# Optimization experiments

Hardware: AMD Instinct MI355X
Metric: run time of the kernel (lower is better)

Reference implementation:

```python
import jax, jax.numpy as jnp
import numpy as np

B, N, FD, HD, MD, FS, NM = 8, 64, 128, 256, 64, 80, 6
D = HD + MD  # 320: GNN/decoder operating dim (fixes dim bug in original)
H = W = 128

def _mlp2(x, W1, b1, W2, b2):
    return jax.nn.relu(jax.nn.relu(x @ W1 + b1) @ W2 + b2)

def _forward(object_features, object_attributes, perception_features, object_positions,
             enc_W1, enc_b1, enc_W2, enc_b2, conv1_W, conv1_b, conv2_W, conv2_b,
             edge_W1, edge_b1, edge_W2, edge_b2, gru_Wih, gru_Whh, gru_bih, gru_bhh,
             mode_W1, mode_b1, mode_W2, mode_b2, traj_W1, traj_b1, traj_W2, traj_b2):
    # object encoder: [B,N,FD+8] -> [B,N,HD]
    obj_in = jnp.concatenate([object_features, object_attributes], -1)
    emb = _mlp2(obj_in, enc_W1, enc_b1, enc_W2, enc_b2)
    # map encoder (original discards result via random sampler; kept for faithfulness)
    dn = ('NCHW', 'OIHW', 'NCHW')
    m = jax.nn.relu(jax.lax.conv_general_dilated(perception_features, conv1_W, (1, 1), 'SAME', dimension_numbers=dn) + conv1_b[None, :, None, None])
    m = jax.nn.relu(jax.lax.conv_general_dilated(m, conv2_W, (1, 1), 'SAME', dimension_numbers=dn) + conv2_b[None, :, None, None])
    # sample_map_at_positions returns randn in the original; fixed-seed equivalent
    sampled = jax.random.normal(jax.random.key(42), (B, N, MD), dtype=emb.dtype)
    ctx = jnp.concatenate([emb, sampled], -1)  # [B,N,D]
    # Social GNN, fully vectorized over the ego-node loop i:
    rel = object_positions[:, :, None, :] - object_positions[:, None, :, :]  # [B,N,N,2] = pos[i]-pos[j]
    ego = jnp.broadcast_to(ctx[:, :, None, :], (B, N, N, D))
    nbr = jnp.broadcast_to(ctx[:, None, :, :], (B, N, N, D))
    e = _mlp2(jnp.concatenate([ego, nbr, rel], -1), edge_W1, edge_b1, edge_W2, edge_b2)  # [B,N,N,D]
    mask = (1.0 - jnp.eye(N, dtype=e.dtype))[None, :, :, None]
    agg = (e * mask).sum(2) / (N - 1 + 1e-10)  # [B,N,D]
    # GRUCell(input=concat(ctx,agg), hidden=ctx), torch semantics
    x = jnp.concatenate([ctx, agg], -1)  # [B,N,2D]
    gi = x @ gru_Wih + gru_bih
    gh = ctx @ gru_Whh + gru_bhh
    ir, iz, inn = jnp.split(gi, 3, -1)
    hr, hz, hn = jnp.split(gh, 3, -1)
    r = jax.nn.sigmoid(ir + hr)
    z = jax.nn.sigmoid(iz + hz)
    n = jnp.tanh(inn + r * hn)
    h = (1.0 - z) * n + z * ctx  # [B,N,D]
    # multi-modal trajectory decoder
    mode_probs = jax.nn.softmax(jax.nn.relu(h @ mode_W1 + mode_b1) @ mode_W2 + mode_b2, -1)  # [B,N,NM]
    t = jax.nn.relu(jnp.einsum('bnd,mde->bnme', h, traj_W1) + traj_b1)  # [B,N,NM,D]
    traj = jnp.einsum('bnme,mef->bnmf', t, traj_W2) + traj_b2  # [B,N,NM,FS*2]
    traj = traj.reshape(B, N, NM, FS, 2)
    return traj, mode_probs

def setup_inputs() -> dict:
    key = jax.random.key(0)
    ks = jax.random.split(key, 24)
    p = lambda k, shape: jax.random.normal(k, shape, dtype=jnp.float32) * 0.02
    z = lambda *shape: jnp.zeros(shape, dtype=jnp.float32)
    return {
        'object_features': jax.random.normal(ks[0], (B, N, FD), dtype=jnp.float32),
        'object_attributes': jax.random.normal(ks[1], (B, N, 8), dtype=jnp.float32),
        'perception_features': jax.random.normal(ks[2], (B, 256, H, W), dtype=jnp.float32),
        'object_positions': jax.random.normal(ks[3], (B, N, 2), dtype=jnp.float32),
        'enc_W1': p(ks[4], (FD + 8, HD)), 'enc_b1': z(HD),
        'enc_W2': p(ks[5], (HD, HD)), 'enc_b2': z(HD),
        'conv1_W': p(ks[6], (128, 256, 3, 3)), 'conv1_b': z(128),
        'conv2_W': p(ks[7], (64, 128, 3, 3)), 'conv2_b': z(64),
        'edge_W1': p(ks[8], (2 * D + 2, D)), 'edge_b1': z(D),
        'edge_W2': p(ks[9], (D, D)), 'edge_b2': z(D),
        'gru_Wih': p(ks[10], (2 * D, 3 * D)), 'gru_Whh': p(ks[11], (D, 3 * D)),
        'gru_bih': z(3 * D), 'gru_bhh': z(3 * D),
        'mode_W1': p(ks[12], (D, D)), 'mode_b1': z(D),
        'mode_W2': p(ks[13], (D, NM)), 'mode_b2': z(NM),
        'traj_W1': p(ks[14], (NM, D, D)), 'traj_b1': z(NM, D),
        'traj_W2': p(ks[15], (NM, D, FS * 2)), 'traj_b2': z(NM, FS * 2),
    }

def reference(object_features, object_attributes, perception_features, object_positions,
              enc_W1, enc_b1, enc_W2, enc_b2, conv1_W, conv1_b, conv2_W, conv2_b,
              edge_W1, edge_b1, edge_W2, edge_b2, gru_Wih, gru_Whh, gru_bih, gru_bhh,
              mode_W1, mode_b1, mode_W2, mode_b2, traj_W1, traj_b1, traj_W2, traj_b2):
    return _forward(object_features, object_attributes, perception_features, object_positions,
                    enc_W1, enc_b1, enc_W2, enc_b2, conv1_W, conv1_b, conv2_W, conv2_b,
                    edge_W1, edge_b1, edge_W2, edge_b2, gru_Wih, gru_Whh, gru_bih, gru_bhh,
                    mode_W1, mode_b1, mode_W2, mode_b2, traj_W1, traj_b1, traj_W2, traj_b2)
```

## Files before the change

kernel.cpp:

```cpp
#include <hip/hip_runtime.h>


typedef __attribute__((ext_vector_type(8))) short bf16x8;
typedef __attribute__((ext_vector_type(4))) float f32x4;

__device__ __forceinline__ unsigned short f2bf(float x) {
  unsigned u = __float_as_uint(x);
  return (unsigned short)((u + 0x7fffu + ((u >> 16) & 1u)) >> 16);
}

__device__ __forceinline__ void threefry2x32(unsigned k0, unsigned k1,
                                             unsigned& x0, unsigned& x1) {
  const unsigned ks0 = k0, ks1 = k1, ks2 = k0 ^ k1 ^ 0x1BD11BDAu;
  x0 += ks0; x1 += ks1;
#define TFR(r) { x0 += x1; x1 = (x1 << (r)) | (x1 >> (32 - (r))); x1 ^= x0; }
  TFR(13) TFR(15) TFR(26) TFR(6)  x0 += ks1; x1 += ks2 + 1u;
  TFR(17) TFR(29) TFR(16) TFR(24) x0 += ks2; x1 += ks0 + 2u;
  TFR(13) TFR(15) TFR(26) TFR(6)  x0 += ks0; x1 += ks1 + 3u;
  TFR(17) TFR(29) TFR(16) TFR(24) x0 += ks1; x1 += ks2 + 4u;
  TFR(13) TFR(15) TFR(26) TFR(6)  x0 += ks2; x1 += ks0 + 5u;
#undef TFR
}

__device__ __forceinline__ float erfinv_xla(float x) {
  float w = -logf((1.0f - x) * (1.0f + x));
  float p;
  if (w < 5.0f) {
    w = w - 2.5f;
    p = 2.81022636e-08f;
    p = fmaf(p, w, 3.43273939e-07f);
    p = fmaf(p, w, -3.5233877e-06f);
    p = fmaf(p, w, -4.39150654e-06f);
    p = fmaf(p, w, 0.00021858087f);
    p = fmaf(p, w, -0.00125372503f);
    p = fmaf(p, w, -0.00417768164f);
    p = fmaf(p, w, 0.246640727f);
    p = fmaf(p, w, 1.50140941f);
  } else {
    w = sqrtf(w) - 3.0f;
    p = -0.000200214257f;
    p = fmaf(p, w, 0.000100950558f);
    p = fmaf(p, w, 0.00134934322f);
    p = fmaf(p, w, -0.00367342844f);
    p = fmaf(p, w, 0.00573950773f);
    p = fmaf(p, w, -0.0076224613f);
    p = fmaf(p, w, 0.00943887047f);
    p = fmaf(p, w, 1.00167406f);
    p = fmaf(p, w, 2.83297682f);
  }
  return p * x;
}

__device__ __forceinline__ float jax_normal42(unsigned idx) {
  unsigned x0 = 0u, x1 = idx;
  threefry2x32(0u, 42u, x0, x1);
  unsigned bits = x0 ^ x1;
  float f = __uint_as_float((bits >> 9) | 0x3f800000u) - 1.0f;
  const float lo = -0.99999994f;
  float u = fmaxf(lo, f * 2.0f + lo);
  return 1.41421356237f * erfinv_xla(u);
}

__global__ __launch_bounds__(256)
void k_cvt(const float* __restrict__ W2e, const float* __restrict__ Wih,
           const float* __restrict__ Whh, const float* __restrict__ T1,
           const float* __restrict__ T2, const float* __restrict__ EW1,
           const float* __restrict__ MW1, const float* __restrict__ MW2,
           unsigned short* __restrict__ ub) {
  const int id = blockIdx.x * 256 + threadIdx.x;
  if (id >= 282240) return;
  if (id >= 281600) {
    const int rem = id - 281600;
    const int g = rem >> 4, n = rem & 15;
    unsigned short v[8];
#pragma unroll
    for (int e = 0; e < 8; ++e) v[e] = (n < 6) ? f2bf(MW2[(g * 8 + e) * 6 + n]) : 0;
    ushort4* d = (ushort4*)&ub[2252800 + (size_t)rem * 8];
    d[0] = make_ushort4(v[0], v[1], v[2], v[3]);
    d[1] = make_ushort4(v[4], v[5], v[6], v[7]);
    return;
  }
  const float* src;
  unsigned short* dst;
  int rem, N;
  if (id < 12800)       { src = W2e; dst = ub;           rem = id;          N = 320; }
  else if (id < 89600)  { src = Wih; dst = ub + 102400;  rem = id - 12800;  N = 960; }
  else if (id < 128000) { src = Whh; dst = ub + 716800;  rem = id - 89600;  N = 960; }
  else if (id < 204800) { src = T1;  dst = ub + 1024000; rem = id - 128000; N = 320; }
  else if (id < 243200) { src = T2;  dst = ub + 1638400; rem = id - 204800; N = 160; }
  else if (id < 268800) { src = EW1; dst = ub + 1945600; rem = id - 243200; N = 320; }
  else                  { src = MW1; dst = ub + 2150400; rem = id - 268800; N = 320; }
  const int g = rem / N, n = rem - g * N;
  const float* s = src + g * 8 * N + n;
  unsigned short v[8];
#pragma unroll
  for (int e = 0; e < 8; ++e) v[e] = f2bf(s[e * N]);
  ushort4* d = (ushort4*)&dst[(size_t)rem * 8];
  d[0] = make_ushort4(v[0], v[1], v[2], v[3]);
  d[1] = make_ushort4(v[4], v[5], v[6], v[7]);
}

__global__ __launch_bounds__(256)
void k_encoder(const float* __restrict__ feat, const float* __restrict__ attr,
               const float* __restrict__ W1, const float* __restrict__ b1,
               const float* __restrict__ W2, const float* __restrict__ b2,
               float* __restrict__ ctx) {
  __shared__ float s_in[4][136];
  __shared__ float s_h1[4][256];
  const int r0 = blockIdx.x * 4;
  const int t = threadIdx.x;
  for (int r = 0; r < 4; ++r) {
    if (t < 128)      s_in[r][t] = feat[(r0 + r) * 128 + t];
    else if (t < 136) s_in[r][t] = attr[(r0 + r) * 8 + (t - 128)];
  }
  __syncthreads();
  float acc[4];
#pragma unroll
  for (int r = 0; r < 4; ++r) acc[r] = b1[t];
  for (int k = 0; k < 136; ++k) {
    const float w = W1[k * 256 + t];
#pragma unroll
    for (int r = 0; r < 4; ++r) acc[r] = fmaf(s_in[r][k], w, acc[r]);
  }
#pragma unroll
  for (int r = 0; r < 4; ++r) s_h1[r][t] = fmaxf(acc[r], 0.0f);
  __syncthreads();
#pragma unroll
  for (int r = 0; r < 4; ++r) acc[r] = b2[t];
  for (int k = 0; k < 256; ++k) {
    const float w = W2[k * 256 + t];
#pragma unroll
    for (int r = 0; r < 4; ++r) acc[r] = fmaf(s_h1[r][k], w, acc[r]);
  }
#pragma unroll
  for (int r = 0; r < 4; ++r) ctx[(r0 + r) * 320 + t] = fmaxf(acc[r], 0.0f);
  if (t < 64) {
    for (int r = 0; r < 4; ++r)
      ctx[(r0 + r) * 320 + 256 + t] = jax_normal42((unsigned)((r0 + r) * 64 + t));
  }
}

__global__ __launch_bounds__(256)
void k_pqM(const float* __restrict__ ctx, const unsigned short* __restrict__ Bf,
           const float* __restrict__ b1, float* __restrict__ P,
           float* __restrict__ Q) {
  __shared__ __align__(16) unsigned short s_c[40 * 16 * 8];
  const int row0 = blockIdx.x * 16;
  const int half = blockIdx.y;
  const int t = threadIdx.x;
#pragma unroll
  for (int it = 0; it < 3; ++it) {
    const int idx = t + it * 256;
    if (idx < 640) {
      const int row = idx / 40, oct = idx - row * 40;
      const float4 v0 = *(const float4*)&ctx[(row0 + row) * 320 + oct * 8];
      const float4 v1 = *(const float4*)&ctx[(row0 + row) * 320 + oct * 8 + 4];
      ushort4* dst = (ushort4*)&s_c[(oct * 16 + row) * 8];
      dst[0] = make_ushort4(f2bf(v0.x), f2bf(v0.y), f2bf(v0.z), f2bf(v0.w));
      dst[1] = make_ushort4(f2bf(v1.x), f2bf(v1.y), f2bf(v1.z), f2bf(v1.w));
    }
  }
  __syncthreads();

  const int w = t >> 6, l = t & 63, lg = l >> 4, lr = l & 15;
  f32x4 acc[5];
#pragma unroll
  for (int u = 0; u < 5; ++u) acc[u] = (f32x4){0.f, 0.f, 0.f, 0.f};
#pragma unroll
  for (int ks = 0; ks < 10; ++ks) {
    const bf16x8 afr = *(const bf16x8*)&s_c[((ks * 4 + lg) * 16 + lr) * 8];
    bf16x8 bfr[5];
#pragma unroll
    for (int u = 0; u < 5; ++u)
      bfr[u] = *(const bf16x8*)&Bf[(((ks * 4 + lg) * 640) + half * 320 +
                                    w * 80 + u * 16 + lr) * 8];
#pragma unroll
    for (int u = 0; u < 5; ++u)
      acc[u] = __builtin_amdgcn_mfma_f32_16x16x32_bf16(afr, bfr[u], acc[u], 0, 0, 0);
  }
#pragma unroll
  for (int u = 0; u < 5; ++u) {
    const int n = w * 80 + u * 16 + lr;
    const float bias = (half == 0) ? b1[n] : 0.0f;
    float* dst = (half == 0) ? P : Q;
#pragma unroll
    for (int r = 0; r < 4; ++r) {
      const int row = row0 + lg * 4 + r;
      dst[row * 320 + n] = acc[u][r] + bias;
    }
  }
}

__global__ __launch_bounds__(256)
void k_edge(const float* __restrict__ P, const float* __restrict__ Q,
            const float* __restrict__ pos, const float* __restrict__ W1,
            const unsigned short* __restrict__ Bf, const float* __restrict__ b2,
            float* __restrict__ agg) {
  __shared__ __align__(16) unsigned short s_A[40 * 64 * 8];
  const int bx = blockIdx.x;
  const int b = bx >> 6, i = bx & 63;
  const int t = threadIdx.x;
  const int w = t >> 6, l = t & 63;

  {
    const int j = t & 63;
    const int sub = t >> 6;
    const float2 pi = *(const float2*)&pos[b * 128 + 2 * i];
    const float2 pj = *(const float2*)&pos[b * 128 + 2 * j];
    const float rx = pi.x - pj.x, ry = pi.y - pj.y;
    const float* __restrict__ Prow = P + bx * 320;
    const float* __restrict__ Qrow = Q + (b * 64 + j) * 320;
    const float* __restrict__ w0 = W1 + 640 * 320;
    const float* __restrict__ w1 = W1 + 641 * 320;
#pragma unroll
    for (int g = 0; g < 10; ++g) {
      const int k0 = g * 32 + sub * 8;
      const float4 p0 = *(const float4*)&Prow[k0];
      const float4 p1 = *(const float4*)&Prow[k0 + 4];
      const float4 q0 = *(const float4*)&Qrow[k0];
      const float4 q1 = *(const float4*)&Qrow[k0 + 4];
      const float4 a0 = *(const float4*)&w0[k0];
      const float4 a1 = *(const float4*)&w0[k0 + 4];
      const float4 c0 = *(const float4*)&w1[k0];
      const float4 c1 = *(const float4*)&w1[k0 + 4];
      float v[8];
      v[0] = fmaf(ry, c0.x, fmaf(rx, a0.x, p0.x + q0.x));
      v[1] = fmaf(ry, c0.y, fmaf(rx, a0.y, p0.y + q0.y));
      v[2] = fmaf(ry, c0.z, fmaf(rx, a0.z, p0.z + q0.z));
      v[3] = fmaf(ry, c0.w, fmaf(rx, a0.w, p0.w + q0.w));
      v[4] = fmaf(ry, c1.x, fmaf(rx, a1.x, p1.x + q1.x));
      v[5] = fmaf(ry, c1.y, fmaf(rx, a1.y, p1.y + q1.y));
      v[6] = fmaf(ry, c1.z, fmaf(rx, a1.z, p1.z + q1.z));
      v[7] = fmaf(ry, c1.w, fmaf(rx, a1.w, p1.w + q1.w));
      unsigned short u[8];
#pragma unroll
      for (int e = 0; e < 8; ++e) u[e] = f2bf(fmaxf(v[e], 0.0f));
      ushort4* dst = (ushort4*)&s_A[((g * 4 + sub) * 64 + j) * 8];
      dst[0] = make_ushort4(u[0], u[1], u[2], u[3]);
      dst[1] = make_ushort4(u[4], u[5], u[6], u[7]);
    }
  }
  __syncthreads();

  f32x4 acc[4][5];
#pragma unroll
  for (int mt = 0; mt < 4; ++mt)
#pragma unroll
    for (int u = 0; u < 5; ++u) acc[mt][u] = (f32x4){0.f, 0.f, 0.f, 0.f};

  const int lg = l >> 4, lr = l & 15;
  const unsigned short* __restrict__ Bbase = Bf + (lg * 320 + w * 80 + lr) * 8;
  const unsigned short* __restrict__ Abase = s_A + lg * 512 + lr * 8;

#pragma unroll 2
  for (int ks = 0; ks < 10; ++ks) {
    bf16x8 afr[4];
#pragma unroll
    for (int mt = 0; mt < 4; ++mt)
      afr[mt] = *(const bf16x8*)(Abase + ks * 2048 + mt * 128);
    bf16x8 bfr[5];
#pragma unroll
    for (int u = 0; u < 5; ++u)
      bfr[u] = *(const bf16x8*)(Bbase + ks * 10240 + u * 128);
#pragma unroll
    for (int mt = 0; mt < 4; ++mt)
#pragma unroll
      for (int u = 0; u < 5; ++u)
        acc[mt][u] = __builtin_amdgcn_mfma_f32_16x16x32_bf16(
            afr[mt], bfr[u], acc[mt][u], 0, 0, 0);
  }

#pragma unroll
  for (int u = 0; u < 5; ++u) {
    const int n = w * 80 + u * 16 + lr;
    const float bias = b2[n];
    float p = 0.0f;
#pragma unroll
    for (int mt = 0; mt < 4; ++mt) {
#pragma unroll
      for (int r = 0; r < 4; ++r) {
        const int j = mt * 16 + lg * 4 + r;
        const float e = fmaxf(acc[mt][u][r] + bias, 0.0f);
        p += (j != i) ? e : 0.0f;
      }
    }
    p += __shfl_xor(p, 16);
    p += __shfl_xor(p, 32);
    if (l < 16) agg[bx * 320 + n] = p * (1.0f / 63.0f);
  }
}

__global__ __launch_bounds__(256)
void k_gruM(const float* __restrict__ ctx, const float* __restrict__ agg,
            const unsigned short* __restrict__ BfI,
            const unsigned short* __restrict__ BfH,
            const float* __restrict__ bih, const float* __restrict__ bhh,
            float* __restrict__ h) {
  __shared__ __align__(16) unsigned short s_x[80 * 16 * 8];
  const int rb = blockIdx.x / 5, db = blockIdx.x % 5;
  const int row0 = rb * 16, d0 = db * 64;
  const int t = threadIdx.x;

#pragma unroll
  for (int it = 0; it < 5; ++it) {
    const int idx = t + it * 256;
    const int row = idx / 80, oct = idx - row * 80;
    float4 v0, v1;
    if (oct < 40) {
      v0 = *(const float4*)&ctx[(row0 + row) * 320 + oct * 8];
      v1 = *(const float4*)&ctx[(row0 + row) * 320 + oct * 8 + 4];
    } else {
      v0 = *(const float4*)&agg[(row0 + row) * 320 + (oct - 40) * 8];
      v1 = *(const float4*)&agg[(row0 + row) * 320 + (oct - 40) * 8 + 4];
    }
    ushort4* dst = (ushort4*)&s_x[(oct * 16 + row) * 8];
    dst[0] = make_ushort4(f2bf(v0.x), f2bf(v0.y), f2bf(v0.z), f2bf(v0.w));
    dst[1] = make_ushort4(f2bf(v1.x), f2bf(v1.y), f2bf(v1.z), f2bf(v1.w));
  }
  __syncthreads();

  const int w = t >> 6, l = t & 63, lg = l >> 4, lr = l & 15;
  const int d = d0 + w * 16 + lr;

  f32x4 accI[3], accH[3];
#pragma unroll
  for (int g = 0; g < 3; ++g) {
    accI[g] = (f32x4){0.f, 0.f, 0.f, 0.f};
    accH[g] = (f32x4){0.f, 0.f, 0.f, 0.f};
  }

#pragma unroll 2
  for (int ks = 0; ks < 20; ++ks) {
    const bf16x8 afr = *(const bf16x8*)&s_x[((ks * 4 + lg) * 16 + lr) * 8];
    bf16x8 bfr[3];
#pragma unroll
    for (int g = 0; g < 3; ++g)
      bfr[g] = *(const bf16x8*)&BfI[((ks * 4 + lg) * 960 + g * 320 + d) * 8];
#pragma unroll
    for (int g = 0; g < 3; ++g)
      accI[g] = __builtin_amdgcn_mfma_f32_16x16x32_bf16(afr, bfr[g], accI[g], 0, 0, 0);
  }
#pragma unroll 2
  for (int ks = 0; ks < 10; ++ks) {
    const bf16x8 afr = *(const bf16x8*)&s_x[((ks * 4 + lg) * 16 + lr) * 8];
    bf16x8 bfr[3];
#pragma unroll
    for (int g = 0; g < 3; ++g)
      bfr[g] = *(const bf16x8*)&BfH[((ks * 4 + lg) * 960 + g * 320 + d) * 8];
#pragma unroll
    for (int g = 0; g < 3; ++g)
      accH[g] = __builtin_amdgcn_mfma_f32_16x16x32_bf16(afr, bfr[g], accH[g], 0, 0, 0);
  }

  const float b_ir = bih[d], b_iz = bih[320 + d], b_in = bih[640 + d];
  const float b_hr = bhh[d], b_hz = bhh[320 + d], b_hn = bhh[640 + d];
#pragma unroll
  for (int r = 0; r < 4; ++r) {
    const int row = row0 + lg * 4 + r;
    const float ir = accI[0][r] + b_ir;
    const float iz = accI[1][r] + b_iz;
    const float inn = accI[2][r] + b_in;
    const float hr = accH[0][r] + b_hr;
    const float hz = accH[1][r] + b_hz;
    const float hn = accH[2][r] + b_hn;
    const float rr = 1.0f / (1.0f + expf(-(ir + hr)));
    const float zz = 1.0f / (1.0f + expf(-(iz + hz)));
    const float nn = tanhf(fmaf(rr, hn, inn));
    const float c = ctx[row * 320 + d];
    h[row * 320 + d] = (1.0f - zz) * nn + zz * c;
  }
}

__global__ __launch_bounds__(256)
void k_modeM(const float* __restrict__ h, const unsigned short* __restrict__ B1,
             const float* __restrict__ b1, const unsigned short* __restrict__ B2,
             const float* __restrict__ b2, float* __restrict__ out) {
  __shared__ __align__(16) unsigned short s_h[40 * 32 * 8];
  __shared__ __align__(16) unsigned short s_t[40 * 32 * 8];
  __shared__ float s_l[32][6];
  const int row0 = blockIdx.x * 32;
  const int t = threadIdx.x;

#pragma unroll
  for (int it = 0; it < 5; ++it) {
    const int idx = t + it * 256;
    const int row = idx / 40, oct = idx - row * 40;
    const float4 v0 = *(const float4*)&h[(row0 + row) * 320 + oct * 8];
    const float4 v1 = *(const float4*)&h[(row0 + row) * 320 + oct * 8 + 4];
    ushort4* dst = (ushort4*)&s_h[(oct * 32 + row) * 8];
    dst[0] = make_ushort4(f2bf(v0.x), f2bf(v0.y), f2bf(v0.z), f2bf(v0.w));
    dst[1] = make_ushort4(f2bf(v1.x), f2bf(v1.y), f2bf(v1.z), f2bf(v1.w));
  }
  __syncthreads();

  const int w = t >> 6, l = t & 63, lg = l >> 4, lr = l & 15;

  f32x4 acc1[2][5];
#pragma unroll
  for (int mt = 0; mt < 2; ++mt)
#pragma unroll
    for (int u = 0; u < 5; ++u) acc1[mt][u] = (f32x4){0.f, 0.f, 0.f, 0.f};
#pragma unroll
  for (int ks = 0; ks < 10; ++ks) {
    bf16x8 afr[2];
#pragma unroll
    for (int mt = 0; mt < 2; ++mt)
      afr[mt] = *(const bf16x8*)&s_h[(((ks * 4 + lg) * 32) + mt * 16 + lr) * 8];
    bf16x8 bfr[5];
#pragma unroll
    for (int u = 0; u < 5; ++u)
      bfr[u] = *(const bf16x8*)&B1[((ks * 4 + lg) * 320 + w * 80 + u * 16 + lr) * 8];
#pragma unroll
    for (int mt = 0; mt < 2; ++mt)
#pragma unroll
      for (int u = 0; u < 5; ++u)
        acc1[mt][u] = __builtin_amdgcn_mfma_f32_16x16x32_bf16(
            afr[mt], bfr[u], acc1[mt][u], 0, 0, 0);
  }
#pragma unroll
  for (int u = 0; u < 5; ++u) {
    const int n = w * 80 + u * 16 + lr;
    const float bias = b1[n];
#pragma unroll
    for (int mt = 0; mt < 2; ++mt) {
#pragma unroll
      for (int r = 0; r < 4; ++r) {
        const int row = mt * 16 + lg * 4 + r;
        s_t[((n >> 3) * 32 + row) * 8 + (n & 7)] =
            f2bf(fmaxf(acc1[mt][u][r] + bias, 0.0f));
      }
    }
  }
  __syncthreads();

  if (w < 2) {
    f32x4 acc2 = (f32x4){0.f, 0.f, 0.f, 0.f};
#pragma unroll
    for (int ks = 0; ks < 10; ++ks) {
      const bf16x8 afr = *(const bf16x8*)&s_t[(((ks * 4 + lg) * 32) + w * 16 + lr) * 8];
      const bf16x8 bfr = *(const bf16x8*)&B2[((ks * 4 + lg) * 16 + lr) * 8];
      acc2 = __builtin_amdgcn_mfma_f32_16x16x32_bf16(afr, bfr, acc2, 0, 0, 0);
    }
    if (lr < 6) {
#pragma unroll
      for (int r = 0; r < 4; ++r)
        s_l[w * 16 + lg * 4 + r][lr] = acc2[r] + b2[lr];
    }
  }
  __syncthreads();

  if (t < 32) {
    float v[6];
#pragma unroll
    for (int q = 0; q < 6; ++q) v[q] = s_l[t][q];
    float mx = v[0];
#pragma unroll
    for (int q = 1; q < 6; ++q) mx = fmaxf(mx, v[q]);
    float sum = 0.0f;
#pragma unroll
    for (int q = 0; q < 6; ++q) { v[q] = expf(v[q] - mx); sum += v[q]; }
    const float inv = 1.0f / sum;
#pragma unroll
    for (int q = 0; q < 6; ++q) out[491520 + (row0 + t) * 6 + q] = v[q] * inv;
  }
}

__global__ __launch_bounds__(256)
void k_trajM(const float* __restrict__ h, const unsigned short* __restrict__ B1,
             const float* __restrict__ b1, const unsigned short* __restrict__ B2,
             const float* __restrict__ b2, float* __restrict__ out) {
  __shared__ __align__(16) unsigned short s_h[40 * 16 * 8];
  __shared__ __align__(16) unsigned short s_t[40 * 16 * 8];
  const int rb = blockIdx.x, m = blockIdx.y;
  const int row0 = rb * 16;
  const int t = threadIdx.x;

#pragma unroll
  for (int it = 0; it < 3; ++it) {
    const int idx = t + it * 256;
    if (idx < 640) {
      const int row = idx / 40, oct = idx - row * 40;
      const float4 v0 = *(const float4*)&h[(row0 + row) * 320 + oct * 8];
      const float4 v1 = *(const float4*)&h[(row0 + row) * 320 + oct * 8 + 4];
      ushort4* dst = (ushort4*)&s_h[(oct * 16 + row) * 8];
      dst[0] = make_ushort4(f2bf(v0.x), f2bf(v0.y), f2bf(v0.z), f2bf(v0.w));
      dst[1] = make_ushort4(f2bf(v1.x), f2bf(v1.y), f2bf(v1.z), f2bf(v1.w));
    }
  }
  __syncthreads();

  const int w = t >> 6, l = t & 63, lg = l >> 4, lr = l & 15;

  f32x4 acc1[5];
#pragma unroll
  for (int u = 0; u < 5; ++u) acc1[u] = (f32x4){0.f, 0.f, 0.f, 0.f};
  const unsigned short* __restrict__ B1m = B1 + m * 102400;
#pragma unroll
  for (int ks = 0; ks < 10; ++ks) {
    const bf16x8 afr = *(const bf16x8*)&s_h[((ks * 4 + lg) * 16 + lr) * 8];
    bf16x8 bfr[5];
#pragma unroll
    for (int u = 0; u < 5; ++u)
      bfr[u] = *(const bf16x8*)&B1m[((ks * 4 + lg) * 320 + w * 80 + u * 16 + lr) * 8];
#pragma unroll
    for (int u = 0; u < 5; ++u)
      acc1[u] = __builtin_amdgcn_mfma_f32_16x16x32_bf16(afr, bfr[u], acc1[u], 0, 0, 0);
  }
#pragma unroll
  for (int u = 0; u < 5; ++u) {
    const int n = w * 80 + u * 16 + lr;
    const float bias = b1[m * 320 + n];
#pragma unroll
    for (int r = 0; r < 4; ++r) {
      const int row = lg * 4 + r;
      s_t[((n >> 3) * 16 + row) * 8 + (n & 7)] =
          f2bf(fmaxf(acc1[u][r] + bias, 0.0f));
    }
  }
  __syncthreads();

  const int nb = (w == 0) ? 0 : (w == 1) ? 3 : (w == 2) ? 6 : 7;
  f32x4 acc2[3];
#pragma unroll
  for (int u = 0; u < 3; ++u) acc2[u] = (f32x4){0.f, 0.f, 0.f, 0.f};
  const unsigned short* __restrict__ B2m = B2 + m * 51200;
#pragma unroll
  for (int ks = 0; ks < 10; ++ks) {
    const bf16x8 afr = *(const bf16x8*)&s_t[((ks * 4 + lg) * 16 + lr) * 8];
    bf16x8 bfr[3];
#pragma unroll
    for (int u = 0; u < 3; ++u)
      bfr[u] = *(const bf16x8*)&B2m[((ks * 4 + lg) * 160 + (nb + u) * 16 + lr) * 8];
#pragma unroll
    for (int u = 0; u < 3; ++u)
      acc2[u] = __builtin_amdgcn_mfma_f32_16x16x32_bf16(afr, bfr[u], acc2[u], 0, 0, 0);
  }
#pragma unroll
  for (int u = 0; u < 3; ++u) {
    const int n = (nb + u) * 16 + lr;
    const float bias = b2[m * 160 + n];
#pragma unroll
    for (int r = 0; r < 4; ++r) {
      const int row = row0 + lg * 4 + r;
      out[(row * 6 + m) * 160 + n] = acc2[u][r] + bias;
    }
  }
}

extern "C" void kernel_launch(void* const* d_in, const int* in_sizes, int n_in,
                              void* d_out, int out_size, void* d_ws, size_t ws_size,
                              hipStream_t stream) {
  (void)in_sizes; (void)n_in; (void)out_size; (void)ws_size;
  const float* feat  = (const float*)d_in[0];
  const float* attr  = (const float*)d_in[1];
  const float* pos   = (const float*)d_in[3];
  const float* encW1 = (const float*)d_in[4];
  const float* encb1 = (const float*)d_in[5];
  const float* encW2 = (const float*)d_in[6];
  const float* encb2 = (const float*)d_in[7];
  const float* edgW1 = (const float*)d_in[12];
  const float* edgb1 = (const float*)d_in[13];
  const float* edgW2 = (const float*)d_in[14];
  const float* edgb2 = (const float*)d_in[15];
  const float* Wih   = (const float*)d_in[16];
  const float* Whh   = (const float*)d_in[17];
  const float* bih   = (const float*)d_in[18];
  const float* bhh   = (const float*)d_in[19];
  const float* mW1   = (const float*)d_in[20];
  const float* mb1   = (const float*)d_in[21];
  const float* mW2   = (const float*)d_in[22];
  const float* mb2   = (const float*)d_in[23];
  const float* tW1   = (const float*)d_in[24];
  const float* tb1   = (const float*)d_in[25];
  const float* tW2   = (const float*)d_in[26];
  const float* tb2   = (const float*)d_in[27];

  float* out = (float*)d_out;
  float* ws  = (float*)d_ws;
  float* ctx  = ws;
  float* P    = ws + 163840;
  float* Q    = ws + 327680;
  float* agg  = ws + 491520;
  float* hbuf = ws + 655360;
  unsigned short* ub = (unsigned short*)(ws + 819200);
  unsigned short* W2bf  = ub;
  unsigned short* WihBf = ub + 102400;
  unsigned short* WhhBf = ub + 716800;
  unsigned short* T1bf  = ub + 1024000;
  unsigned short* T2bf  = ub + 1638400;
  unsigned short* EW1bf = ub + 1945600;
  unsigned short* MW1bf = ub + 2150400;
  unsigned short* MW2bf = ub + 2252800;

  k_cvt<<<1103, 256, 0, stream>>>(edgW2, Wih, Whh, tW1, tW2, edgW1, mW1, mW2, ub);
  k_encoder<<<128, 256, 0, stream>>>(feat, attr, encW1, encb1, encW2, encb2, ctx);
  k_pqM<<<dim3(32, 2), 256, 0, stream>>>(ctx, EW1bf, edgb1, P, Q);
  k_edge<<<512, 256, 0, stream>>>(P, Q, pos, edgW1, W2bf, edgb2, agg);
  k_gruM<<<160, 256, 0, stream>>>(ctx, agg, WihBf, WhhBf, bih, bhh, hbuf);
  k_modeM<<<16, 256, 0, stream>>>(hbuf, MW1bf, mb1, MW2bf, mb2, out);
  k_trajM<<<dim3(32, 6), 256, 0, stream>>>(hbuf, T1bf, tb1, T2bf, tb2, out);
}
```

Before: 87.48 us.

## Merge independent kernels and swizzle edge A-tile LDS layout

Merges the weight-conversion and encoder kernels into one launch, and the mode and trajectory head kernels into another. The goal is to cut launch overhead and let independent work run side by side. The edge kernel now fills its staging tile in a row-contiguous order that coalesces Q loads, and XOR-swizzles the shared-memory layout to reduce bank conflicts on the MFMA operand reads. The merged kernels share one shared-memory footprint sized for the larger branch, which may lower occupancy for the smaller branch.

```diff
diff --git a/kernel.cpp b/kernel.cpp
--- a/kernel.cpp
+++ b/kernel.cpp
@@ -62,53 +62,55 @@
 }
 
 __global__ __launch_bounds__(256)
-void k_cvt(const float* __restrict__ W2e, const float* __restrict__ Wih,
-           const float* __restrict__ Whh, const float* __restrict__ T1,
-           const float* __restrict__ T2, const float* __restrict__ EW1,
-           const float* __restrict__ MW1, const float* __restrict__ MW2,
-           unsigned short* __restrict__ ub) {
-  const int id = blockIdx.x * 256 + threadIdx.x;
-  if (id >= 282240) return;
-  if (id >= 281600) {
-    const int rem = id - 281600;
-    const int g = rem >> 4, n = rem & 15;
+void k_head(const float* __restrict__ W2e, const float* __restrict__ Wih,
+            const float* __restrict__ Whh, const float* __restrict__ T1,
+            const float* __restrict__ T2, const float* __restrict__ EW1,
+            const float* __restrict__ MW1, const float* __restrict__ MW2,
+            unsigned short* __restrict__ ub,
+            const float* __restrict__ feat, const float* __restrict__ attr,
+            const float* __restrict__ eW1, const float* __restrict__ eb1,
+            const float* __restrict__ eW2, const float* __restrict__ eb2,
+            float* __restrict__ ctx) {
+  __shared__ float s_in[4][136];
+  __shared__ float s_h1[4][256];
+  const int t = threadIdx.x;
+
+  if (blockIdx.x < 1103) {
+    const int id = blockIdx.x * 256 + t;
+    if (id >= 282240) return;
+    if (id >= 281600) {
+      const int rem = id - 281600;
+      const int g = rem >> 4, n = rem & 15;
+      unsigned short v[8];
+#pragma unroll
+      for (int e = 0; e < 8; ++e) v[e] = (n < 6) ? f2bf(MW2[(g * 8 + e) * 6 + n]) : 0;
+      ushort4* d = (ushort4*)&ub[2252800 + (size_t)rem * 8];
+      d[0] = make_ushort4(v[0], v[1], v[2], v[3]);
+      d[1] = make_ushort4(v[4], v[5], v[6], v[7]);
+      return;
+    }
+    const float* src;
+    unsigned short* dst;
+    int rem, N;
+    if (id < 12800)       { src = W2e; dst = ub;           rem = id;          N = 320; }
+    else if (id < 89600)  { src = Wih; dst = ub + 102400;  rem = id - 12800;  N = 960; }
+    else if (id < 128000) { src = Whh; dst = ub + 716800;  rem = id - 89600;  N = 960; }
+    else if (id < 204800) { src = T1;  dst = ub + 1024000; rem = id - 128000; N = 320; }
+    else if (id < 243200) { src = T2;  dst = ub + 1638400; rem = id - 204800; N = 160; }
+    else if (id < 268800) { src = EW1; dst = ub + 1945600; rem = id - 243200; N = 320; }
+    else                  { src = MW1; dst = ub + 2150400; rem = id - 268800; N = 320; }
+    const int g = rem / N, n = rem - g * N;
+    const float* s = src + g * 8 * N + n;
     unsigned short v[8];
 #pragma unroll
-    for (int e = 0; e < 8; ++e) v[e] = (n < 6) ? f2bf(MW2[(g * 8 + e) * 6 + n]) : 0;
-    ushort4* d = (ushort4*)&ub[2252800 + (size_t)rem * 8];
+    for (int e = 0; e < 8; ++e) v[e] = f2bf(s[e * N]);
+    ushort4* d = (ushort4*)&dst[(size_t)rem * 8];
     d[0] = make_ushort4(v[0], v[1], v[2], v[3]);
     d[1] = make_ushort4(v[4], v[5], v[6], v[7]);
     return;
   }
-  const float* src;
-  unsigned short* dst;
-  int rem, N;
-  if (id < 12800)       { src = W2e; dst = ub;           rem = id;          N = 320; }
-  else if (id < 89600)  { src = Wih; dst = ub + 102400;  rem = id - 12800;  N = 960; }
-  else if (id < 128000) { src = Whh; dst = ub + 716800;  rem = id - 89600;  N = 960; }
-  else if (id < 204800) { src = T1;  dst = ub + 1024000; rem = id - 128000; N = 320; }
-  else if (id < 243200) { src = T2;  dst = ub + 1638400; rem = id - 204800; N = 160; }
-  else if (id < 268800) { src = EW1; dst = ub + 1945600; rem = id - 243200; N = 320; }
-  else                  { src = MW1; dst = ub + 2150400; rem = id - 268800; N = 320; }
-  const int g = rem / N, n = rem - g * N;
-  const float* s = src + g * 8 * N + n;
-  unsigned short v[8];
-#pragma unroll
-  for (int e = 0; e < 8; ++e) v[e] = f2bf(s[e * N]);
-  ushort4* d = (ushort4*)&dst[(size_t)rem * 8];
-  d[0] = make_ushort4(v[0], v[1], v[2], v[3]);
-  d[1] = make_ushort4(v[4], v[5], v[6], v[7]);
-}
-
-__global__ __launch_bounds__(256)
-void k_encoder(const float* __restrict__ feat, const float* __restrict__ attr,
-               const float* __restrict__ W1, const float* __restrict__ b1,
-               const float* __restrict__ W2, const float* __restrict__ b2,
-               float* __restrict__ ctx) {
-  __shared__ float s_in[4][136];
-  __shared__ float s_h1[4][256];
-  const int r0 = blockIdx.x * 4;
-  const int t = threadIdx.x;
+
+  const int r0 = (blockIdx.x - 1103) * 4;
   for (int r = 0; r < 4; ++r) {
     if (t < 128)      s_in[r][t] = feat[(r0 + r) * 128 + t];
     else if (t < 136) s_in[r][t] = attr[(r0 + r) * 8 + (t - 128)];
@@ -116,9 +118,9 @@
   __syncthreads();
   float acc[4];
 #pragma unroll
-  for (int r = 0; r < 4; ++r) acc[r] = b1[t];
+  for (int r = 0; r < 4; ++r) acc[r] = eb1[t];
   for (int k = 0; k < 136; ++k) {
-    const float w = W1[k * 256 + t];
+    const float w = eW1[k * 256 + t];
 #pragma unroll
     for (int r = 0; r < 4; ++r) acc[r] = fmaf(s_in[r][k], w, acc[r]);
   }
@@ -126,9 +128,9 @@
   for (int r = 0; r < 4; ++r) s_h1[r][t] = fmaxf(acc[r], 0.0f);
   __syncthreads();
 #pragma unroll
-  for (int r = 0; r < 4; ++r) acc[r] = b2[t];
+  for (int r = 0; r < 4; ++r) acc[r] = eb2[t];
   for (int k = 0; k < 256; ++k) {
-    const float w = W2[k * 256 + t];
+    const float w = eW2[k * 256 + t];
 #pragma unroll
     for (int r = 0; r < 4; ++r) acc[r] = fmaf(s_h1[r][k], w, acc[r]);
   }
@@ -203,22 +205,23 @@
   const int w = t >> 6, l = t & 63;
 
   {
-    const int j = t & 63;
-    const int sub = t >> 6;
     const float2 pi = *(const float2*)&pos[b * 128 + 2 * i];
-    const float2 pj = *(const float2*)&pos[b * 128 + 2 * j];
-    const float rx = pi.x - pj.x, ry = pi.y - pj.y;
     const float* __restrict__ Prow = P + bx * 320;
-    const float* __restrict__ Qrow = Q + (b * 64 + j) * 320;
     const float* __restrict__ w0 = W1 + 640 * 320;
     const float* __restrict__ w1 = W1 + 641 * 320;
 #pragma unroll
-    for (int g = 0; g < 10; ++g) {
-      const int k0 = g * 32 + sub * 8;
+    for (int it = 0; it < 10; ++it) {
+      const int tau = w * 640 + it * 64 + l;
+      const int j = tau / 40;
+      const int oct = tau - j * 40;
+      const int k0 = oct * 8;
+      const float2 pj = *(const float2*)&pos[b * 128 + 2 * j];
+      const float rx = pi.x - pj.x, ry = pi.y - pj.y;
+      const float* __restrict__ Qrow = Q + (b * 64 + j) * 320;
+      const float4 q0 = *(const float4*)&Qrow[k0];
+      const float4 q1 = *(const float4*)&Qrow[k0 + 4];
       const float4 p0 = *(const float4*)&Prow[k0];
       const float4 p1 = *(const float4*)&Prow[k0 + 4];
-      const float4 q0 = *(const float4*)&Qrow[k0];
-      const float4 q1 = *(const float4*)&Qrow[k0 + 4];
       const float4 a0 = *(const float4*)&w0[k0];
       const float4 a1 = *(const float4*)&w0[k0 + 4];
       const float4 c0 = *(const float4*)&w1[k0];
@@ -235,9 +238,9 @@
       unsigned short u[8];
 #pragma unroll
       for (int e = 0; e < 8; ++e) u[e] = f2bf(fmaxf(v[e], 0.0f));
-      ushort4* dst = (ushort4*)&s_A[((g * 4 + sub) * 64 + j) * 8];
-      dst[0] = make_ushort4(u[0], u[1], u[2], u[3]);
-      dst[1] = make_ushort4(u[4], u[5], u[6], u[7]);
+      const int swz = ((oct * 64 + j) * 8) ^ ((oct & 7) << 3);
+      *(ushort4*)&s_A[swz]     = make_ushort4(u[0], u[1], u[2], u[3]);
+      *(ushort4*)&s_A[swz + 4] = make_ushort4(u[4], u[5], u[6], u[7]);
     }
   }
   __syncthreads();
@@ -250,14 +253,16 @@
 
   const int lg = l >> 4, lr = l & 15;
   const unsigned short* __restrict__ Bbase = Bf + (lg * 320 + w * 80 + lr) * 8;
-  const unsigned short* __restrict__ Abase = s_A + lg * 512 + lr * 8;
 
 #pragma unroll 2
   for (int ks = 0; ks < 10; ++ks) {
+    const int oct = ks * 4 + lg;
     bf16x8 afr[4];
 #pragma unroll
-    for (int mt = 0; mt < 4; ++mt)
-      afr[mt] = *(const bf16x8*)(Abase + ks * 2048 + mt * 128);
+    for (int mt = 0; mt < 4; ++mt) {
+      const int elem = ((oct * 64 + mt * 16 + lr) * 8) ^ ((oct & 7) << 3);
+      afr[mt] = *(const bf16x8*)&s_A[elem];
+    }
     bf16x8 bfr[5];
 #pragma unroll
     for (int u = 0; u < 5; ++u)
@@ -372,108 +377,108 @@
 }
 
 __global__ __launch_bounds__(256)
-void k_modeM(const float* __restrict__ h, const unsigned short* __restrict__ B1,
-             const float* __restrict__ b1, const unsigned short* __restrict__ B2,
-             const float* __restrict__ b2, float* __restrict__ out) {
-  __shared__ __align__(16) unsigned short s_h[40 * 32 * 8];
-  __shared__ __align__(16) unsigned short s_t[40 * 32 * 8];
+void k_tail(const float* __restrict__ h, const unsigned short* __restrict__ MB1,
+            const float* __restrict__ mb1, const unsigned short* __restrict__ MB2,
+            const float* __restrict__ mb2, const unsigned short* __restrict__ TB1,
+            const float* __restrict__ tb1, const unsigned short* __restrict__ TB2,
+            const float* __restrict__ tb2, float* __restrict__ out) {
+  __shared__ __align__(16) unsigned short s_buf[20480];
   __shared__ float s_l[32][6];
-  const int row0 = blockIdx.x * 32;
   const int t = threadIdx.x;
-
-#pragma unroll
-  for (int it = 0; it < 5; ++it) {
-    const int idx = t + it * 256;
-    const int row = idx / 40, oct = idx - row * 40;
-    const float4 v0 = *(const float4*)&h[(row0 + row) * 320 + oct * 8];
-    const float4 v1 = *(const float4*)&h[(row0 + row) * 320 + oct * 8 + 4];
-    ushort4* dst = (ushort4*)&s_h[(oct * 32 + row) * 8];
-    dst[0] = make_ushort4(f2bf(v0.x), f2bf(v0.y), f2bf(v0.z), f2bf(v0.w));
-    dst[1] = make_ushort4(f2bf(v1.x), f2bf(v1.y), f2bf(v1.z), f2bf(v1.w));
-  }
-  __syncthreads();
-
   const int w = t >> 6, l = t & 63, lg = l >> 4, lr = l & 15;
 
-  f32x4 acc1[2][5];
-#pragma unroll
-  for (int mt = 0; mt < 2; ++mt)
-#pragma unroll
-    for (int u = 0; u < 5; ++u) acc1[mt][u] = (f32x4){0.f, 0.f, 0.f, 0.f};
-#pragma unroll
-  for (int ks = 0; ks < 10; ++ks) {
-    bf16x8 afr[2];
+  if (blockIdx.x < 16) {
+    unsigned short* s_h = s_buf;
+    unsigned short* s_t = s_buf + 10240;
+    const int row0 = blockIdx.x * 32;
+#pragma unroll
+    for (int it = 0; it < 5; ++it) {
+      const int idx = t + it * 256;
+      const int row = idx / 40, oct = idx - row * 40;
+      const float4 v0 = *(const float4*)&h[(row0 + row) * 320 + oct * 8];
+      const float4 v1 = *(const float4*)&h[(row0 + row) * 320 + oct * 8 + 4];
+      ushort4* dst = (ushort4*)&s_h[(oct * 32 + row) * 8];
+      dst[0] = make_ushort4(f2bf(v0.x), f2bf(v0.y), f2bf(v0.z), f2bf(v0.w));
+      dst[1] = make_ushort4(f2bf(v1.x), f2bf(v1.y), f2bf(v1.z), f2bf(v1.w));
+    }
+    __syncthreads();
+
+    f32x4 acc1[2][5];
 #pragma unroll
     for (int mt = 0; mt < 2; ++mt)
-      afr[mt] = *(const bf16x8*)&s_h[(((ks * 4 + lg) * 32) + mt * 16 + lr) * 8];
-    bf16x8 bfr[5];
-#pragma unroll
-    for (int u = 0; u < 5; ++u)
-      bfr[u] = *(const bf16x8*)&B1[((ks * 4 + lg) * 320 + w * 80 + u * 16 + lr) * 8];
-#pragma unroll
-    for (int mt = 0; mt < 2; ++mt)
+#pragma unroll
+      for (int u = 0; u < 5; ++u) acc1[mt][u] = (f32x4){0.f, 0.f, 0.f, 0.f};
+#pragma unroll
+    for (int ks = 0; ks < 10; ++ks) {
+      bf16x8 afr[2];
+#pragma unroll
+      for (int mt = 0; mt < 2; ++mt)
+        afr[mt] = *(const bf16x8*)&s_h[(((ks * 4 + lg) * 32) + mt * 16 + lr) * 8];
+      bf16x8 bfr[5];
 #pragma unroll
       for (int u = 0; u < 5; ++u)
-        acc1[mt][u] = __builtin_amdgcn_mfma_f32_16x16x32_bf16(
-            afr[mt], bfr[u], acc1[mt][u], 0, 0, 0);
-  }
-#pragma unroll
-  for (int u = 0; u < 5; ++u) {
-    const int n = w * 80 + u * 16 + lr;
-    const float bias = b1[n];
-#pragma unroll
-    for (int mt = 0; mt < 2; ++mt) {
-#pragma unroll
-      for (int r = 0; r < 4; ++r) {
-        const int row = mt * 16 + lg * 4 + r;
-        s_t[((n >> 3) * 32 + row) * 8 + (n & 7)] =
-            f2bf(fmaxf(acc1[mt][u][r] + bias, 0.0f));
+        bfr[u] = *(const bf16x8*)&MB1[((ks * 4 + lg) * 320 + w * 80 + u * 16 + lr) * 8];
+#pragma unroll
+      for (int mt = 0; mt < 2; ++mt)
+#pragma unroll
+        for (int u = 0; u < 5; ++u)
+          acc1[mt][u] = __builtin_amdgcn_mfma_f32_16x16x32_bf16(
+              afr[mt], bfr[u], acc1[mt][u], 0, 0, 0);
+    }
+#pragma unroll
+    for (int u = 0; u < 5; ++u) {
+      const int n = w * 80 + u * 16 + lr;
+      const float bias = mb1[n];
+#pragma unroll
+      for (int mt = 0; mt < 2; ++mt) {
+#pragma unroll
+        for (int r = 0; r < 4; ++r) {
+          const int row = mt * 16 + lg * 4 + r;
+          s_t[((n >> 3) * 32 + row) * 8 + (n & 7)] =
+              f2bf(fmaxf(acc1[mt][u][r] + bias, 0.0f));
+        }
       }
     }
-  }
-  __syncthreads();
-
-  if (w < 2) {
-    f32x4 acc2 = (f32x4){0.f, 0.f, 0.f, 0.f};
-#pragma unroll
-    for (int ks = 0; ks < 10; ++ks) {
-      const bf16x8 afr = *(const bf16x8*)&s_t[(((ks * 4 + lg) * 32) + w * 16 + lr) * 8];
-      const bf16x8 bfr = *(const bf16x8*)&B2[((ks * 4 + lg) * 16 + lr) * 8];
-      acc2 = __builtin_amdgcn_mfma_f32_16x16x32_bf16(afr, bfr, acc2, 0, 0, 0);
-    }
-    if (lr < 6) {
-#pragma unroll
-      for (int r = 0; r < 4; ++r)
-        s_l[w * 16 + lg * 4 + r][lr] = acc2[r] + b2[lr];
-    }
-  }
-  __syncthreads();
-
-  if (t < 32) {
-    float v[6];
-#pragma unroll
-    for (int q = 0; q < 6; ++q) v[q] = s_l[t][q];
-    float mx = v[0];
-#pragma unroll
-    for (int q = 1; q < 6; ++q) mx = fmaxf(mx, v[q]);
-    float sum = 0.0f;
-#pragma unroll
-    for (int q = 0; q < 6; ++q) { v[q] = expf(v[q] - mx); sum += v[q]; }
-    const float inv = 1.0f / sum;
-#pragma unroll
-    for (int q = 0; q < 6; ++q) out[491520 + (row0 + t) * 6 + q] = v[q] * inv;
-  }
-}
-
-__global__ __launch_bounds__(256)
-void k_trajM(const float* __restrict__ h, const unsigned short* __restrict__ B1,
-             const float* __restrict__ b1, const unsigned short* __restrict__ B2,
-             const float* __restrict__ b2, float* __restrict__ out) {
-  __shared__ __align__(16) unsigned short s_h[40 * 16 * 8];
-  __shared__ __align__(16) unsigned short s_t[40 * 16 * 8];
-  const int rb = blockIdx.x, m = blockIdx.y;
+    __syncthreads();
+
+    if (w < 2) {
+      f32x4 acc2 = (f32x4){0.f, 0.f, 0.f, 0.f};
+#pragma unroll
+      for (int ks = 0; ks < 10; ++ks) {
+        const bf16x8 afr = *(const bf16x8*)&s_t[(((ks * 4 + lg) * 32) + w * 16 + lr) * 8];
+        const bf16x8 bfr = *(const bf16x8*)&MB2[((ks * 4 + lg) * 16 + lr) * 8];
+        acc2 = __builtin_amdgcn_mfma_f32_16x16x32_bf16(afr, bfr, acc2, 0, 0, 0);
+      }
+      if (lr < 6) {
+#pragma unroll
+        for (int r = 0; r < 4; ++r)
+          s_l[w * 16 + lg * 4 + r][lr] = acc2[r] + mb2[lr];
+      }
+    }
+    __syncthreads();
+
+    if (t < 32) {
+      float v[6];
+#pragma unroll
+      for (int q = 0; q < 6; ++q) v[q] = s_l[t][q];
+      float mx = v[0];
+#pragma unroll
+      for (int q = 1; q < 6; ++q) mx = fmaxf(mx, v[q]);
+      float sum = 0.0f;
+#pragma unroll
+      for (int q = 0; q < 6; ++q) { v[q] = expf(v[q] - mx); sum += v[q]; }
+      const float inv = 1.0f / sum;
+#pragma unroll
+      for (int q = 0; q < 6; ++q) out[491520 + (row0 + t) * 6 + q] = v[q] * inv;
+    }
+    return;
+  }
+
+  const int idx0 = blockIdx.x - 16;
+  const int m = idx0 >> 5, rb = idx0 & 31;
+  unsigned short* s_h = s_buf;
+  unsigned short* s_t = s_buf + 5120;
   const int row0 = rb * 16;
-  const int t = threadIdx.x;
 
 #pragma unroll
   for (int it = 0; it < 3; ++it) {
@@ -489,12 +494,10 @@
   }
   __syncthreads();
 
-  const int w = t >> 6, l = t & 63, lg = l >> 4, lr = l & 15;
-
   f32x4 acc1[5];
 #pragma unroll
   for (int u = 0; u < 5; ++u) acc1[u] = (f32x4){0.f, 0.f, 0.f, 0.f};
-  const unsigned short* __restrict__ B1m = B1 + m * 102400;
+  const unsigned short* __restrict__ B1m = TB1 + m * 102400;
 #pragma unroll
   for (int ks = 0; ks < 10; ++ks) {
     const bf16x8 afr = *(const bf16x8*)&s_h[((ks * 4 + lg) * 16 + lr) * 8];
@@ -509,7 +512,7 @@
 #pragma unroll
   for (int u = 0; u < 5; ++u) {
     const int n = w * 80 + u * 16 + lr;
-    const float bias = b1[m * 320 + n];
+    const float bias = tb1[m * 320 + n];
 #pragma unroll
     for (int r = 0; r < 4; ++r) {
       const int row = lg * 4 + r;
@@ -523,7 +526,7 @@
   f32x4 acc2[3];
 #pragma unroll
   for (int u = 0; u < 3; ++u) acc2[u] = (f32x4){0.f, 0.f, 0.f, 0.f};
-  const unsigned short* __restrict__ B2m = B2 + m * 51200;
+  const unsigned short* __restrict__ B2m = TB2 + m * 51200;
 #pragma unroll
   for (int ks = 0; ks < 10; ++ks) {
     const bf16x8 afr = *(const bf16x8*)&s_t[((ks * 4 + lg) * 16 + lr) * 8];
@@ -538,7 +541,7 @@
 #pragma unroll
   for (int u = 0; u < 3; ++u) {
     const int n = (nb + u) * 16 + lr;
-    const float bias = b2[m * 160 + n];
+    const float bias = tb2[m * 160 + n];
 #pragma unroll
     for (int r = 0; r < 4; ++r) {
       const int row = row0 + lg * 4 + r;
@@ -592,11 +595,11 @@
   unsigned short* MW1bf = ub + 2150400;
   unsigned short* MW2bf = ub + 2252800;
 
-  k_cvt<<<1103, 256, 0, stream>>>(edgW2, Wih, Whh, tW1, tW2, edgW1, mW1, mW2, ub);
-  k_encoder<<<128, 256, 0, stream>>>(feat, attr, encW1, encb1, encW2, encb2, ctx);
+  k_head<<<1231, 256, 0, stream>>>(edgW2, Wih, Whh, tW1, tW2, edgW1, mW1, mW2, ub,
+                                   feat, attr, encW1, encb1, encW2, encb2, ctx);
   k_pqM<<<dim3(32, 2), 256, 0, stream>>>(ctx, EW1bf, edgb1, P, Q);
   k_edge<<<512, 256, 0, stream>>>(P, Q, pos, edgW1, W2bf, edgb2, agg);
   k_gruM<<<160, 256, 0, stream>>>(ctx, agg, WihBf, WhhBf, bih, bhh, hbuf);
-  k_modeM<<<16, 256, 0, stream>>>(hbuf, MW1bf, mb1, MW2bf, mb2, out);
-  k_trajM<<<dim3(32, 6), 256, 0, stream>>>(hbuf, T1bf, tb1, T2bf, tb2, out);
-}
+  k_tail<<<208, 256, 0, stream>>>(hbuf, MW1bf, mb1, MW2bf, mb2,
+                                  T1bf, tb1, T2bf, tb2, out);
+}
```

After: 78.35 us (median of 2 runs). 10.4% less time.
